# Performance work log

Hardware: AMD Instinct MI355X
Metric: run time of the kernel (lower is better)

## Reference

```python
import jax, jax.numpy as jnp
import numpy as np

TEMP = 2.0   # NTXent uses a hardcoded temperature of 2, not the ctor's 0.07
EPS = 1e-8   # F.cosine_similarity eps


def setup_inputs() -> dict:
    key = jax.random.key(0)
    k1, _ = jax.random.split(key)
    x = jax.random.normal(k1, (8192, 256), dtype=jnp.float32)
    unused = jnp.zeros((1,), dtype=jnp.int32)
    return {"x": x, "unused": unused}


def _cos_matrix(a, b):
    # pairwise cosine similarity: [N, N]
    na = jnp.linalg.norm(a, axis=-1)
    nb = jnp.linalg.norm(b, axis=-1)
    dots = a @ b.T
    return dots / jnp.maximum(na[:, None] * nb[None, :], EPS)


def reference(x, unused):
    n = x.shape[0] // 2
    p, q = x[:n], x[n:]  # anchor, positive

    s_pp = _cos_matrix(p, p)
    s_pn = _cos_matrix(p, q)
    s_nn = _cos_matrix(q, q)
    s_np = _cos_matrix(q, p)

    # double loop i, j in [i, n): upper triangle including diagonal
    mask = jnp.triu(jnp.ones((n, n), dtype=bool))

    exp_sum = (jnp.exp(s_pp / TEMP) + jnp.exp(s_pn / TEMP)
               + jnp.exp(s_nn / TEMP) + jnp.exp(s_np / TEMP))
    sim_all = jnp.sum(jnp.where(mask, exp_sum, 0.0))

    sim_s = jnp.sum(jnp.exp(jnp.diagonal(s_pn) / TEMP))

    return -jnp.log(sim_s / sim_all)
```

## Files before the change

### kernel.cpp

```cpp
#include <hip/hip_runtime.h>

#define DIM    256
#define NROWS  8192
#define NHALF  4096
#define NTILE  64
#define NBLK   ((NTILE * (NTILE + 1)) / 2)

using i32x4  = __attribute__((ext_vector_type(4))) int;
using i32x8  = __attribute__((ext_vector_type(8))) int;
using f32x16 = __attribute__((ext_vector_type(16))) float;

struct i32x8_pair { i32x4 lo, hi; };

__global__ __launch_bounds__(256) void normalize_k(const float* __restrict__ x,
                                                   unsigned char* __restrict__ z8) {
  const int row  = blockIdx.x * 4 + (threadIdx.x >> 6);
  const int lane = threadIdx.x & 63;
  float4 v = ((const float4*)(x + (size_t)row * DIM))[lane];
  float ss = v.x * v.x + v.y * v.y + v.z * v.z + v.w * v.w;
#pragma unroll
  for (int off = 32; off > 0; off >>= 1) ss += __shfl_xor(ss, off, 64);
  float rn = rsqrtf(fmaxf(ss, 1e-24f));
  int p = __builtin_amdgcn_cvt_pk_fp8_f32(v.x * rn, v.y * rn, 0, false);
  p     = __builtin_amdgcn_cvt_pk_fp8_f32(v.z * rn, v.w * rn, p, true);
  ((int*)(z8 + (size_t)row * DIM))[lane] = p;
}

__global__ __launch_bounds__(256, 3) void gram_k(const unsigned char* __restrict__ z8,
                                                 double2* __restrict__ partial) {
  __shared__ unsigned char As[128 * 128];
  __shared__ unsigned char Bs[128 * 128];
  __shared__ float red[8];

  const int bid = blockIdx.x;
  int bi = (int)((129.0 - sqrt(129.0 * 129.0 - 8.0 * (double)bid)) * 0.5);
  while ((bi * (129 - bi)) / 2 > bid) --bi;
  while (((bi + 1) * (128 - bi)) / 2 <= bid) ++bi;
  const int bj = bi + (bid - (bi * (129 - bi)) / 2);

  const int tid   = threadIdx.x;
  const int lane  = tid & 63;
  const int w     = tid >> 6;
  const int wr    = w >> 1, wc = w & 1;
  const int l31   = lane & 31;
  const int khalf = lane >> 5;

  const size_t rowA0 = (size_t)bi * 128;
  const size_t rowB0 = (size_t)bj * 128;

  f32x16 acc_f[2][2] = {};

  for (int kb = 0; kb < 2; ++kb) {
#pragma unroll
    for (int i = 0; i < 4; ++i) {
      int c   = i * 256 + tid;
      int row = c >> 3;
      int cb  = c & 7;
      int gcb = cb ^ (row & 7);
      const unsigned char* ga = z8 + (rowA0 + row) * DIM + kb * 128 + gcb * 16;
      const unsigned char* gb = z8 + (rowB0 + row) * DIM + kb * 128 + gcb * 16;
      __builtin_amdgcn_global_load_lds(
          (const __attribute__((address_space(1))) void*)ga,
          (__attribute__((address_space(3))) void*)&As[(size_t)(i * 256 + (tid & ~63)) * 16],
          16, 0, 0);
      __builtin_amdgcn_global_load_lds(
          (const __attribute__((address_space(1))) void*)gb,
          (__attribute__((address_space(3))) void*)&Bs[(size_t)(i * 256 + (tid & ~63)) * 16],
          16, 0, 0);
    }
    __syncthreads();

#pragma unroll
    for (int kc = 0; kc < 2; ++kc) {
      i32x8 a[2], b[2];
#pragma unroll
      for (int t = 0; t < 2; ++t) {
        const int cb0 = kc * 4 + khalf * 2;
        int mr = wr * 64 + t * 32 + l31;
        i32x8_pair pa = { *(const i32x4*)&As[mr * 128 + ((cb0    ) ^ (mr & 7)) * 16],
                          *(const i32x4*)&As[mr * 128 + ((cb0 + 1) ^ (mr & 7)) * 16] };
        a[t] = __builtin_bit_cast(i32x8, pa);
        int nr = wc * 64 + t * 32 + l31;
        i32x8_pair pb = { *(const i32x4*)&Bs[nr * 128 + ((cb0    ) ^ (nr & 7)) * 16],
                          *(const i32x4*)&Bs[nr * 128 + ((cb0 + 1) ^ (nr & 7)) * 16] };
        b[t] = __builtin_bit_cast(i32x8, pb);
      }
#pragma unroll
      for (int ti = 0; ti < 2; ++ti)
#pragma unroll
        for (int tj = 0; tj < 2; ++tj)
          acc_f[ti][tj] = __builtin_amdgcn_mfma_scale_f32_32x32x64_f8f6f4(
              a[ti], b[tj], acc_f[ti][tj],
              0, 0,
              0, 0x7f7f7f7f,
              0, 0x7f7f7f7f);
    }
    __syncthreads();
  }

  const bool tdiag = (bi == bj);
  const bool sdiag = (bj == bi + 32);
  float lsum = 0.0f, dsum = 0.0f;
  if (tdiag || sdiag) {
#pragma unroll
    for (int ti = 0; ti < 2; ++ti)
#pragma unroll
      for (int tj = 0; tj < 2; ++tj)
#pragma unroll
        for (int r = 0; r < 16; ++r) {
          float e = __expf(acc_f[ti][tj][r] * 0.5f);
          lsum += e;
          int row_l = (r & 3) + 8 * (r >> 2) + 4 * khalf;
          if (wr == wc && ti == tj && row_l == l31) dsum += e;
        }
  } else {
#pragma unroll
    for (int ti = 0; ti < 2; ++ti)
#pragma unroll
      for (int tj = 0; tj < 2; ++tj)
#pragma unroll
        for (int r = 0; r < 16; ++r)
          lsum += __expf(acc_f[ti][tj][r] * 0.5f);
  }
#pragma unroll
  for (int off = 32; off > 0; off >>= 1) lsum += __shfl_xor(lsum, off, 64);
  if (tdiag || sdiag) {
#pragma unroll
    for (int off = 32; off > 0; off >>= 1) dsum += __shfl_xor(dsum, off, 64);
  }
  if (lane == 0) { red[w] = lsum; red[4 + w] = dsum; }
  __syncthreads();

  if (tid == 0) {
    float l  = red[0] + red[1] + red[2] + red[3];
    float dd = red[4] + red[5] + red[6] + red[7];
    double2 v;
    v.x = tdiag ? (double)l + (double)dd : 2.0 * (double)l;
    v.y = sdiag ? (double)dd : 0.0;
    partial[bid] = v;
  }
}

__global__ __launch_bounds__(256) void reduce_k(const double2* __restrict__ partial,
                                                float* __restrict__ out) {
  __shared__ double redS[4], redD[4];
  double s = 0.0, ss = 0.0;
  for (int i = threadIdx.x; i < NBLK; i += 256) {
    double2 v = partial[i];
    s += v.x; ss += v.y;
  }
#pragma unroll
  for (int off = 32; off > 0; off >>= 1) {
    s  += __shfl_xor(s,  off, 64);
    ss += __shfl_xor(ss, off, 64);
  }
  const int w = threadIdx.x >> 6;
  if ((threadIdx.x & 63) == 0) { redS[w] = s; redD[w] = ss; }
  __syncthreads();
  if (threadIdx.x == 0) {
    double S  = redS[0] + redS[1] + redS[2] + redS[3];
    double sd = redD[0] + redD[1] + redD[2] + redD[3];
    out[0] = (float)(log(0.5 * S + sd) - log(sd));
  }
}

extern "C" void kernel_launch(void* const* d_in, const int* in_sizes, int n_in,
                              void* d_out, int out_size, void* d_ws, size_t ws_size,
                              hipStream_t stream) {
  const float* x    = (const float*)d_in[0];
  unsigned char* z8 = (unsigned char*)d_ws;
  double2* partial  = (double2*)((char*)d_ws + (size_t)NROWS * DIM);
  float* out        = (float*)d_out;

  normalize_k<<<dim3(NROWS / 4), dim3(256), 0, stream>>>(x, z8);
  gram_k<<<dim3(NBLK), dim3(256), 0, stream>>>(z8, partial);
  reduce_k<<<dim3(1), dim3(256), 0, stream>>>(partial, out);
}
```

Before: 78.45 us.

## Fuse normalize, gram and reduce into one persistent cooperative kernel

After: 147.5 us. 88.0% more time.

```diff
diff --git a/kernel.cpp b/kernel.cpp
--- a/kernel.cpp
+++ b/kernel.cpp
@@ -1,10 +1,14 @@
 #include <hip/hip_runtime.h>
+#include <hip/hip_cooperative_groups.h>
+
+namespace cg = cooperative_groups;
 
 #define DIM    256
 #define NROWS  8192
 #define NHALF  4096
 #define NTILE  64
 #define NBLK   ((NTILE * (NTILE + 1)) / 2)
+#define MAXGRID 696
 
 using i32x4  = __attribute__((ext_vector_type(4))) int;
 using i32x8  = __attribute__((ext_vector_type(8))) int;
@@ -12,31 +16,15 @@
 
 struct i32x8_pair { i32x4 lo, hi; };
 
-__global__ __launch_bounds__(256) void normalize_k(const float* __restrict__ x,
-                                                   unsigned char* __restrict__ z8) {
-  const int row  = blockIdx.x * 4 + (threadIdx.x >> 6);
-  const int lane = threadIdx.x & 63;
-  float4 v = ((const float4*)(x + (size_t)row * DIM))[lane];
-  float ss = v.x * v.x + v.y * v.y + v.z * v.z + v.w * v.w;
-#pragma unroll
-  for (int off = 32; off > 0; off >>= 1) ss += __shfl_xor(ss, off, 64);
-  float rn = rsqrtf(fmaxf(ss, 1e-24f));
-  int p = __builtin_amdgcn_cvt_pk_fp8_f32(v.x * rn, v.y * rn, 0, false);
-  p     = __builtin_amdgcn_cvt_pk_fp8_f32(v.z * rn, v.w * rn, p, true);
-  ((int*)(z8 + (size_t)row * DIM))[lane] = p;
-}
-
-__global__ __launch_bounds__(256, 3) void gram_k(const unsigned char* __restrict__ z8,
-                                                 double2* __restrict__ partial) {
+__global__ __launch_bounds__(256, 3) void fused_k(const float* __restrict__ x,
+                                                  unsigned char* __restrict__ z8,
+                                                  double2* __restrict__ partial,
+                                                  float* __restrict__ out) {
+  cg::grid_group grid = cg::this_grid();
+
   __shared__ unsigned char As[128 * 128];
   __shared__ unsigned char Bs[128 * 128];
   __shared__ float red[8];
-
-  const int bid = blockIdx.x;
-  int bi = (int)((129.0 - sqrt(129.0 * 129.0 - 8.0 * (double)bid)) * 0.5);
-  while ((bi * (129 - bi)) / 2 > bid) --bi;
-  while (((bi + 1) * (128 - bi)) / 2 <= bid) ++bi;
-  const int bj = bi + (bid - (bi * (129 - bi)) / 2);
 
   const int tid   = threadIdx.x;
   const int lane  = tid & 63;
@@ -45,122 +33,148 @@
   const int l31   = lane & 31;
   const int khalf = lane >> 5;
 
-  const size_t rowA0 = (size_t)bi * 128;
-  const size_t rowB0 = (size_t)bj * 128;
-
-  f32x16 acc_f[2][2] = {};
-
-  for (int kb = 0; kb < 2; ++kb) {
-#pragma unroll
-    for (int i = 0; i < 4; ++i) {
-      int c   = i * 256 + tid;
-      int row = c >> 3;
-      int cb  = c & 7;
-      int gcb = cb ^ (row & 7);
-      const unsigned char* ga = z8 + (rowA0 + row) * DIM + kb * 128 + gcb * 16;
-      const unsigned char* gb = z8 + (rowB0 + row) * DIM + kb * 128 + gcb * 16;
-      __builtin_amdgcn_global_load_lds(
-          (const __attribute__((address_space(1))) void*)ga,
-          (__attribute__((address_space(3))) void*)&As[(size_t)(i * 256 + (tid & ~63)) * 16],
-          16, 0, 0);
-      __builtin_amdgcn_global_load_lds(
-          (const __attribute__((address_space(1))) void*)gb,
-          (__attribute__((address_space(3))) void*)&Bs[(size_t)(i * 256 + (tid & ~63)) * 16],
-          16, 0, 0);
-    }
+  for (int row = blockIdx.x * 4 + w; row < NROWS; row += gridDim.x * 4) {
+    float4 v = ((const float4*)(x + (size_t)row * DIM))[lane];
+    float ss = v.x * v.x + v.y * v.y + v.z * v.z + v.w * v.w;
+#pragma unroll
+    for (int off = 32; off > 0; off >>= 1) ss += __shfl_xor(ss, off, 64);
+    float rn = rsqrtf(fmaxf(ss, 1e-24f));
+    int p = __builtin_amdgcn_cvt_pk_fp8_f32(v.x * rn, v.y * rn, 0, false);
+    p     = __builtin_amdgcn_cvt_pk_fp8_f32(v.z * rn, v.w * rn, p, true);
+    ((int*)(z8 + (size_t)row * DIM))[lane] = p;
+  }
+
+  grid.sync();
+
+  double Sloc = 0.0, ssloc = 0.0;
+  for (int bid = blockIdx.x; bid < NBLK; bid += gridDim.x) {
+    int bi = (int)((129.0 - sqrt(129.0 * 129.0 - 8.0 * (double)bid)) * 0.5);
+    while ((bi * (129 - bi)) / 2 > bid) --bi;
+    while (((bi + 1) * (128 - bi)) / 2 <= bid) ++bi;
+    const int bj = bi + (bid - (bi * (129 - bi)) / 2);
+
+    const size_t rowA0 = (size_t)bi * 128;
+    const size_t rowB0 = (size_t)bj * 128;
+
+    f32x16 acc_f[2][2] = {};
+
+    for (int kb = 0; kb < 2; ++kb) {
+#pragma unroll
+      for (int i = 0; i < 4; ++i) {
+        int c   = i * 256 + tid;
+        int row = c >> 3;
+        int cb  = c & 7;
+        int gcb = cb ^ (row & 7);
+        const unsigned char* ga = z8 + (rowA0 + row) * DIM + kb * 128 + gcb * 16;
+        const unsigned char* gb = z8 + (rowB0 + row) * DIM + kb * 128 + gcb * 16;
+        __builtin_amdgcn_global_load_lds(
+            (const __attribute__((address_space(1))) void*)ga,
+            (__attribute__((address_space(3))) void*)&As[(size_t)(i * 256 + (tid & ~63)) * 16],
+            16, 0, 0);
+        __builtin_amdgcn_global_load_lds(
+            (const __attribute__((address_space(1))) void*)gb,
+            (__attribute__((address_space(3))) void*)&Bs[(size_t)(i * 256 + (tid & ~63)) * 16],
+            16, 0, 0);
+      }
+      __syncthreads();
+
+#pragma unroll
+      for (int kc = 0; kc < 2; ++kc) {
+        i32x8 a[2], b[2];
+#pragma unroll
+        for (int t = 0; t < 2; ++t) {
+          const int cb0 = kc * 4 + khalf * 2;
+          int mr = wr * 64 + t * 32 + l31;
+          i32x8_pair pa = { *(const i32x4*)&As[mr * 128 + ((cb0    ) ^ (mr & 7)) * 16],
+                            *(const i32x4*)&As[mr * 128 + ((cb0 + 1) ^ (mr & 7)) * 16] };
+          a[t] = __builtin_bit_cast(i32x8, pa);
+          int nr = wc * 64 + t * 32 + l31;
+          i32x8_pair pb = { *(const i32x4*)&Bs[nr * 128 + ((cb0    ) ^ (nr & 7)) * 16],
+                            *(const i32x4*)&Bs[nr * 128 + ((cb0 + 1) ^ (nr & 7)) * 16] };
+          b[t] = __builtin_bit_cast(i32x8, pb);
+        }
+#pragma unroll
+        for (int ti = 0; ti < 2; ++ti)
+#pragma unroll
+          for (int tj = 0; tj < 2; ++tj)
+            acc_f[ti][tj] = __builtin_amdgcn_mfma_scale_f32_32x32x64_f8f6f4(
+                a[ti], b[tj], acc_f[ti][tj],
+                0, 0,
+                0, 0x7f7f7f7f,
+                0, 0x7f7f7f7f);
+      }
+      __syncthreads();
+    }
+
+    const bool tdiag = (bi == bj);
+    const bool sdiag = (bj == bi + 32);
+    float lsum = 0.0f, dsum = 0.0f;
+    if (tdiag || sdiag) {
+#pragma unroll
+      for (int ti = 0; ti < 2; ++ti)
+#pragma unroll
+        for (int tj = 0; tj < 2; ++tj)
+#pragma unroll
+          for (int r = 0; r < 16; ++r) {
+            float e = __expf(acc_f[ti][tj][r] * 0.5f);
+            lsum += e;
+            int row_l = (r & 3) + 8 * (r >> 2) + 4 * khalf;
+            if (wr == wc && ti == tj && row_l == l31) dsum += e;
+          }
+    } else {
+#pragma unroll
+      for (int ti = 0; ti < 2; ++ti)
+#pragma unroll
+        for (int tj = 0; tj < 2; ++tj)
+#pragma unroll
+          for (int r = 0; r < 16; ++r)
+            lsum += __expf(acc_f[ti][tj][r] * 0.5f);
+    }
+#pragma unroll
+    for (int off = 32; off > 0; off >>= 1) lsum += __shfl_xor(lsum, off, 64);
+    if (tdiag || sdiag) {
+#pragma unroll
+      for (int off = 32; off > 0; off >>= 1) dsum += __shfl_xor(dsum, off, 64);
+    }
+    if (lane == 0) { red[w] = lsum; red[4 + w] = dsum; }
     __syncthreads();
 
-#pragma unroll
-    for (int kc = 0; kc < 2; ++kc) {
-      i32x8 a[2], b[2];
-#pragma unroll
-      for (int t = 0; t < 2; ++t) {
-        const int cb0 = kc * 4 + khalf * 2;
-        int mr = wr * 64 + t * 32 + l31;
-        i32x8_pair pa = { *(const i32x4*)&As[mr * 128 + ((cb0    ) ^ (mr & 7)) * 16],
-                          *(const i32x4*)&As[mr * 128 + ((cb0 + 1) ^ (mr & 7)) * 16] };
-        a[t] = __builtin_bit_cast(i32x8, pa);
-        int nr = wc * 64 + t * 32 + l31;
-        i32x8_pair pb = { *(const i32x4*)&Bs[nr * 128 + ((cb0    ) ^ (nr & 7)) * 16],
-                          *(const i32x4*)&Bs[nr * 128 + ((cb0 + 1) ^ (nr & 7)) * 16] };
-        b[t] = __builtin_bit_cast(i32x8, pb);
-      }
-#pragma unroll
-      for (int ti = 0; ti < 2; ++ti)
-#pragma unroll
-        for (int tj = 0; tj < 2; ++tj)
-          acc_f[ti][tj] = __builtin_amdgcn_mfma_scale_f32_32x32x64_f8f6f4(
-              a[ti], b[tj], acc_f[ti][tj],
-              0, 0,
-              0, 0x7f7f7f7f,
-              0, 0x7f7f7f7f);
+    if (tid == 0) {
+      float l  = red[0] + red[1] + red[2] + red[3];
+      float dd = red[4] + red[5] + red[6] + red[7];
+      Sloc  += tdiag ? (double)l + (double)dd : 2.0 * (double)l;
+      if (sdiag) ssloc += (double)dd;
     }
     __syncthreads();
   }
 
-  const bool tdiag = (bi == bj);
-  const bool sdiag = (bj == bi + 32);
-  float lsum = 0.0f, dsum = 0.0f;
-  if (tdiag || sdiag) {
-#pragma unroll
-    for (int ti = 0; ti < 2; ++ti)
-#pragma unroll
-      for (int tj = 0; tj < 2; ++tj)
-#pragma unroll
-        for (int r = 0; r < 16; ++r) {
-          float e = __expf(acc_f[ti][tj][r] * 0.5f);
-          lsum += e;
-          int row_l = (r & 3) + 8 * (r >> 2) + 4 * khalf;
-          if (wr == wc && ti == tj && row_l == l31) dsum += e;
-        }
-  } else {
-#pragma unroll
-    for (int ti = 0; ti < 2; ++ti)
-#pragma unroll
-      for (int tj = 0; tj < 2; ++tj)
-#pragma unroll
-        for (int r = 0; r < 16; ++r)
-          lsum += __expf(acc_f[ti][tj][r] * 0.5f);
-  }
-#pragma unroll
-  for (int off = 32; off > 0; off >>= 1) lsum += __shfl_xor(lsum, off, 64);
-  if (tdiag || sdiag) {
-#pragma unroll
-    for (int off = 32; off > 0; off >>= 1) dsum += __shfl_xor(dsum, off, 64);
-  }
-  if (lane == 0) { red[w] = lsum; red[4 + w] = dsum; }
-  __syncthreads();
-
   if (tid == 0) {
-    float l  = red[0] + red[1] + red[2] + red[3];
-    float dd = red[4] + red[5] + red[6] + red[7];
-    double2 v;
-    v.x = tdiag ? (double)l + (double)dd : 2.0 * (double)l;
-    v.y = sdiag ? (double)dd : 0.0;
-    partial[bid] = v;
-  }
-}
-
-__global__ __launch_bounds__(256) void reduce_k(const double2* __restrict__ partial,
-                                                float* __restrict__ out) {
-  __shared__ double redS[4], redD[4];
-  double s = 0.0, ss = 0.0;
-  for (int i = threadIdx.x; i < NBLK; i += 256) {
-    double2 v = partial[i];
-    s += v.x; ss += v.y;
-  }
-#pragma unroll
-  for (int off = 32; off > 0; off >>= 1) {
-    s  += __shfl_xor(s,  off, 64);
-    ss += __shfl_xor(ss, off, 64);
-  }
-  const int w = threadIdx.x >> 6;
-  if ((threadIdx.x & 63) == 0) { redS[w] = s; redD[w] = ss; }
-  __syncthreads();
-  if (threadIdx.x == 0) {
-    double S  = redS[0] + redS[1] + redS[2] + redS[3];
-    double sd = redD[0] + redD[1] + redD[2] + redD[3];
-    out[0] = (float)(log(0.5 * S + sd) - log(sd));
+    double2 v; v.x = Sloc; v.y = ssloc;
+    partial[blockIdx.x] = v;
+  }
+
+  grid.sync();
+
+  if (blockIdx.x == 0) {
+    double* redS = (double*)As;
+    double* redD = (double*)Bs;
+    double s = 0.0, ss = 0.0;
+    for (int i = tid; i < (int)gridDim.x; i += 256) {
+      double2 v = partial[i];
+      s += v.x; ss += v.y;
+    }
+#pragma unroll
+    for (int off = 32; off > 0; off >>= 1) {
+      s  += __shfl_xor(s,  off, 64);
+      ss += __shfl_xor(ss, off, 64);
+    }
+    if (lane == 0) { redS[w] = s; redD[w] = ss; }
+    __syncthreads();
+    if (tid == 0) {
+      double S  = redS[0] + redS[1] + redS[2] + redS[3];
+      double sd = redD[0] + redD[1] + redD[2] + redD[3];
+      out[0] = (float)(log(0.5 * S + sd) - log(sd));
+    }
   }
 }
 
@@ -172,7 +186,17 @@
   double2* partial  = (double2*)((char*)d_ws + (size_t)NROWS * DIM);
   float* out        = (float*)d_out;
 
-  normalize_k<<<dim3(NROWS / 4), dim3(256), 0, stream>>>(x, z8);
-  gram_k<<<dim3(NBLK), dim3(256), 0, stream>>>(z8, partial);
-  reduce_k<<<dim3(1), dim3(256), 0, stream>>>(partial, out);
+  static int grid_blocks = 0;
+  if (grid_blocks == 0) {
+    int nb = 0;
+    if (hipOccupancyMaxActiveBlocksPerMultiprocessor(&nb, (const void*)fused_k,
+                                                     256, 0) != hipSuccess || nb < 1)
+      nb = 1;
+    long cap = (long)nb * 256;
+    grid_blocks = (int)(cap < MAXGRID ? cap : MAXGRID);
+  }
+
+  void* args[] = { (void*)&x, (void*)&z8, (void*)&partial, (void*)&out };
+  hipLaunchCooperativeKernel((void*)fused_k, dim3(grid_blocks), dim3(256),
+                             args, 0, stream);
 }
```

## Give each wave its own 64x64 triangular tile and drop block barriers

Applied to the files above, without the earlier changes.

New measurement: 83.59 us. 6.6% more time.

```diff
diff --git a/kernel.cpp b/kernel.cpp
--- a/kernel.cpp
+++ b/kernel.cpp
@@ -3,8 +3,9 @@
 #define DIM    256
 #define NROWS  8192
 #define NHALF  4096
-#define NTILE  64
-#define NBLK   ((NTILE * (NTILE + 1)) / 2)
+#define NT64   128
+#define NWT    ((NT64 * (NT64 + 1)) / 2)
+#define GRID   (NWT / 4)
 
 using i32x4  = __attribute__((ext_vector_type(4))) int;
 using i32x8  = __attribute__((ext_vector_type(8))) int;
@@ -26,63 +27,61 @@
   ((int*)(z8 + (size_t)row * DIM))[lane] = p;
 }
 
-__global__ __launch_bounds__(256, 3) void gram_k(const unsigned char* __restrict__ z8,
+__global__ __launch_bounds__(256, 2) void gram_k(const unsigned char* __restrict__ z8,
                                                  double2* __restrict__ partial) {
-  __shared__ unsigned char As[128 * 128];
-  __shared__ unsigned char Bs[128 * 128];
-  __shared__ float red[8];
-
-  const int bid = blockIdx.x;
-  int bi = (int)((129.0 - sqrt(129.0 * 129.0 - 8.0 * (double)bid)) * 0.5);
-  while ((bi * (129 - bi)) / 2 > bid) --bi;
-  while (((bi + 1) * (128 - bi)) / 2 <= bid) ++bi;
-  const int bj = bi + (bid - (bi * (129 - bi)) / 2);
+  __shared__ unsigned char buf[4][16384];
+  __shared__ double redS[4], redD[4];
 
   const int tid   = threadIdx.x;
   const int lane  = tid & 63;
   const int w     = tid >> 6;
-  const int wr    = w >> 1, wc = w & 1;
   const int l31   = lane & 31;
   const int khalf = lane >> 5;
 
-  const size_t rowA0 = (size_t)bi * 128;
-  const size_t rowB0 = (size_t)bj * 128;
+  const int id = blockIdx.x * 4 + w;
+  int bi = (int)((257.0 - sqrt(257.0 * 257.0 - 8.0 * (double)id)) * 0.5);
+  while ((bi * (257 - bi)) / 2 > id) --bi;
+  while (((bi + 1) * (256 - bi)) / 2 <= id) ++bi;
+  const int bj = bi + (id - (bi * (257 - bi)) / 2);
+
+  const size_t rowA0 = (size_t)bi * 64;
+  const size_t rowB0 = (size_t)bj * 64;
+
+  unsigned char* Aw = &buf[w][0];
+  unsigned char* Bw = &buf[w][8192];
+
+  const int r8 = lane >> 3;
+  const int c8 = lane & 7;
+  const int sw = c8 ^ r8;
 
   f32x16 acc_f[2][2] = {};
 
   for (int kb = 0; kb < 2; ++kb) {
+    const unsigned char* gA = z8 + (rowA0 + r8) * DIM + kb * 128 + sw * 16;
+    const unsigned char* gB = z8 + (rowB0 + r8) * DIM + kb * 128 + sw * 16;
 #pragma unroll
-    for (int i = 0; i < 4; ++i) {
-      int c   = i * 256 + tid;
-      int row = c >> 3;
-      int cb  = c & 7;
-      int gcb = cb ^ (row & 7);
-      const unsigned char* ga = z8 + (rowA0 + row) * DIM + kb * 128 + gcb * 16;
-      const unsigned char* gb = z8 + (rowB0 + row) * DIM + kb * 128 + gcb * 16;
+    for (int g = 0; g < 8; ++g) {
       __builtin_amdgcn_global_load_lds(
-          (const __attribute__((address_space(1))) void*)ga,
-          (__attribute__((address_space(3))) void*)&As[(size_t)(i * 256 + (tid & ~63)) * 16],
-          16, 0, 0);
+          (const __attribute__((address_space(1))) void*)(gA + (size_t)g * 8 * DIM),
+          (__attribute__((address_space(3))) void*)(Aw + g * 1024), 16, 0, 0);
       __builtin_amdgcn_global_load_lds(
-          (const __attribute__((address_space(1))) void*)gb,
-          (__attribute__((address_space(3))) void*)&Bs[(size_t)(i * 256 + (tid & ~63)) * 16],
-          16, 0, 0);
+          (const __attribute__((address_space(1))) void*)(gB + (size_t)g * 8 * DIM),
+          (__attribute__((address_space(3))) void*)(Bw + g * 1024), 16, 0, 0);
     }
-    __syncthreads();
+    __asm__ __volatile__("s_waitcnt vmcnt(0)" ::: "memory");
 
 #pragma unroll
     for (int kc = 0; kc < 2; ++kc) {
+      const int cb0 = kc * 4 + khalf * 2;
       i32x8 a[2], b[2];
 #pragma unroll
       for (int t = 0; t < 2; ++t) {
-        const int cb0 = kc * 4 + khalf * 2;
-        int mr = wr * 64 + t * 32 + l31;
-        i32x8_pair pa = { *(const i32x4*)&As[mr * 128 + ((cb0    ) ^ (mr & 7)) * 16],
-                          *(const i32x4*)&As[mr * 128 + ((cb0 + 1) ^ (mr & 7)) * 16] };
+        int r = t * 32 + l31;
+        i32x8_pair pa = { *(const i32x4*)&Aw[r * 128 + ((cb0    ) ^ (r & 7)) * 16],
+                          *(const i32x4*)&Aw[r * 128 + ((cb0 + 1) ^ (r & 7)) * 16] };
         a[t] = __builtin_bit_cast(i32x8, pa);
-        int nr = wc * 64 + t * 32 + l31;
-        i32x8_pair pb = { *(const i32x4*)&Bs[nr * 128 + ((cb0    ) ^ (nr & 7)) * 16],
-                          *(const i32x4*)&Bs[nr * 128 + ((cb0 + 1) ^ (nr & 7)) * 16] };
+        i32x8_pair pb = { *(const i32x4*)&Bw[r * 128 + ((cb0    ) ^ (r & 7)) * 16],
+                          *(const i32x4*)&Bw[r * 128 + ((cb0 + 1) ^ (r & 7)) * 16] };
         b[t] = __builtin_bit_cast(i32x8, pb);
       }
 #pragma unroll
@@ -95,11 +94,11 @@
               0, 0x7f7f7f7f,
               0, 0x7f7f7f7f);
     }
-    __syncthreads();
+    __asm__ __volatile__("s_waitcnt lgkmcnt(0)" ::: "memory");
   }
 
   const bool tdiag = (bi == bj);
-  const bool sdiag = (bj == bi + 32);
+  const bool sdiag = (bj == bi + 64);
   float lsum = 0.0f, dsum = 0.0f;
   if (tdiag || sdiag) {
 #pragma unroll
@@ -111,7 +110,7 @@
           float e = __expf(acc_f[ti][tj][r] * 0.5f);
           lsum += e;
           int row_l = (r & 3) + 8 * (r >> 2) + 4 * khalf;
-          if (wr == wc && ti == tj && row_l == l31) dsum += e;
+          if (ti == tj && row_l == l31) dsum += e;
         }
   } else {
 #pragma unroll
@@ -128,16 +127,17 @@
 #pragma unroll
     for (int off = 32; off > 0; off >>= 1) dsum += __shfl_xor(dsum, off, 64);
   }
-  if (lane == 0) { red[w] = lsum; red[4 + w] = dsum; }
+
+  if (lane == 0) {
+    redS[w] = tdiag ? (double)lsum + (double)dsum : 2.0 * (double)lsum;
+    redD[w] = sdiag ? (double)dsum : 0.0;
+  }
   __syncthreads();
-
   if (tid == 0) {
-    float l  = red[0] + red[1] + red[2] + red[3];
-    float dd = red[4] + red[5] + red[6] + red[7];
     double2 v;
-    v.x = tdiag ? (double)l + (double)dd : 2.0 * (double)l;
-    v.y = sdiag ? (double)dd : 0.0;
-    partial[bid] = v;
+    v.x = redS[0] + redS[1] + redS[2] + redS[3];
+    v.y = redD[0] + redD[1] + redD[2] + redD[3];
+    partial[blockIdx.x] = v;
   }
 }
 
@@ -145,7 +145,7 @@
                                                 float* __restrict__ out) {
   __shared__ double redS[4], redD[4];
   double s = 0.0, ss = 0.0;
-  for (int i = threadIdx.x; i < NBLK; i += 256) {
+  for (int i = threadIdx.x; i < GRID; i += 256) {
     double2 v = partial[i];
     s += v.x; ss += v.y;
   }
@@ -173,6 +173,6 @@
   float* out        = (float*)d_out;
 
   normalize_k<<<dim3(NROWS / 4), dim3(256), 0, stream>>>(x, z8);
-  gram_k<<<dim3(NBLK), dim3(256), 0, stream>>>(z8, partial);
+  gram_k<<<dim3(GRID), dim3(256), 0, stream>>>(z8, partial);
   reduce_k<<<dim3(1), dim3(256), 0, stream>>>(partial, out);
 }
```

## Quantize normalized rows to FP4 and run Gram matrix with FP4 MFMA

Applied to the files above, without the earlier changes.

Result: faster. 75.20 us (-4.1%).

```diff
diff --git a/kernel.cpp b/kernel.cpp
--- a/kernel.cpp
+++ b/kernel.cpp
@@ -5,6 +5,7 @@
 #define NHALF  4096
 #define NTILE  64
 #define NBLK   ((NTILE * (NTILE + 1)) / 2)
+#define RSTRIDE 128
 
 using i32x4  = __attribute__((ext_vector_type(4))) int;
 using i32x8  = __attribute__((ext_vector_type(8))) int;
@@ -12,24 +13,33 @@
 
 struct i32x8_pair { i32x4 lo, hi; };
 
+__device__ __forceinline__ unsigned fp4q(float v) {
+  float a = fabsf(v);
+  unsigned s = (__builtin_bit_cast(unsigned, v) >> 31) << 3;
+  unsigned c = a < 0.25f ? 0u : a < 0.75f ? 1u : a < 1.25f ? 2u : a < 1.75f ? 3u
+             : a < 2.50f ? 4u : a < 3.50f ? 5u : a < 5.00f ? 6u : 7u;
+  return s | c;
+}
+
 __global__ __launch_bounds__(256) void normalize_k(const float* __restrict__ x,
-                                                   unsigned char* __restrict__ z8) {
+                                                   unsigned char* __restrict__ z4) {
   const int row  = blockIdx.x * 4 + (threadIdx.x >> 6);
   const int lane = threadIdx.x & 63;
   float4 v = ((const float4*)(x + (size_t)row * DIM))[lane];
   float ss = v.x * v.x + v.y * v.y + v.z * v.z + v.w * v.w;
 #pragma unroll
   for (int off = 32; off > 0; off >>= 1) ss += __shfl_xor(ss, off, 64);
-  float rn = rsqrtf(fmaxf(ss, 1e-24f));
-  int p = __builtin_amdgcn_cvt_pk_fp8_f32(v.x * rn, v.y * rn, 0, false);
-  p     = __builtin_amdgcn_cvt_pk_fp8_f32(v.z * rn, v.w * rn, p, true);
-  ((int*)(z8 + (size_t)row * DIM))[lane] = p;
+  float rn = rsqrtf(fmaxf(ss, 1e-24f)) * 16.0f;
+  unsigned c0 = fp4q(v.x * rn), c1 = fp4q(v.y * rn);
+  unsigned c2 = fp4q(v.z * rn), c3 = fp4q(v.w * rn);
+  unsigned short pk = (unsigned short)((c0 | (c1 << 4)) | ((c2 | (c3 << 4)) << 8));
+  ((unsigned short*)(z4 + (size_t)row * RSTRIDE))[lane] = pk;
 }
 
-__global__ __launch_bounds__(256, 3) void gram_k(const unsigned char* __restrict__ z8,
+__global__ __launch_bounds__(256, 4) void gram_k(const unsigned char* __restrict__ z4,
                                                  double2* __restrict__ partial) {
-  __shared__ unsigned char As[128 * 128];
-  __shared__ unsigned char Bs[128 * 128];
+  __shared__ unsigned char As[128 * RSTRIDE];
+  __shared__ unsigned char Bs[128 * RSTRIDE];
   __shared__ float red[8];
 
   const int bid = blockIdx.x;
@@ -48,54 +58,49 @@
   const size_t rowA0 = (size_t)bi * 128;
   const size_t rowB0 = (size_t)bj * 128;
 
+#pragma unroll
+  for (int i = 0; i < 4; ++i) {
+    int c   = i * 256 + tid;
+    int row = c >> 3;
+    int cb  = c & 7;
+    int gcb = cb ^ (row & 7);
+    const unsigned char* ga = z4 + (rowA0 + row) * RSTRIDE + gcb * 16;
+    const unsigned char* gb = z4 + (rowB0 + row) * RSTRIDE + gcb * 16;
+    __builtin_amdgcn_global_load_lds(
+        (const __attribute__((address_space(1))) void*)ga,
+        (__attribute__((address_space(3))) void*)&As[(size_t)(i * 256 + (tid & ~63)) * 16],
+        16, 0, 0);
+    __builtin_amdgcn_global_load_lds(
+        (const __attribute__((address_space(1))) void*)gb,
+        (__attribute__((address_space(3))) void*)&Bs[(size_t)(i * 256 + (tid & ~63)) * 16],
+        16, 0, 0);
+  }
+  __syncthreads();
+
   f32x16 acc_f[2][2] = {};
-
-  for (int kb = 0; kb < 2; ++kb) {
+  const i32x4 zero4 = {0, 0, 0, 0};
 #pragma unroll
-    for (int i = 0; i < 4; ++i) {
-      int c   = i * 256 + tid;
-      int row = c >> 3;
-      int cb  = c & 7;
-      int gcb = cb ^ (row & 7);
-      const unsigned char* ga = z8 + (rowA0 + row) * DIM + kb * 128 + gcb * 16;
-      const unsigned char* gb = z8 + (rowB0 + row) * DIM + kb * 128 + gcb * 16;
-      __builtin_amdgcn_global_load_lds(
-          (const __attribute__((address_space(1))) void*)ga,
-          (__attribute__((address_space(3))) void*)&As[(size_t)(i * 256 + (tid & ~63)) * 16],
-          16, 0, 0);
-      __builtin_amdgcn_global_load_lds(
-          (const __attribute__((address_space(1))) void*)gb,
-          (__attribute__((address_space(3))) void*)&Bs[(size_t)(i * 256 + (tid & ~63)) * 16],
-          16, 0, 0);
+  for (int kc = 0; kc < 4; ++kc) {
+    const int ch = kc * 2 + khalf;
+    i32x8 a[2], b[2];
+#pragma unroll
+    for (int t = 0; t < 2; ++t) {
+      int mr = wr * 64 + t * 32 + l31;
+      i32x8_pair pa = { *(const i32x4*)&As[mr * RSTRIDE + (ch ^ (mr & 7)) * 16], zero4 };
+      a[t] = __builtin_bit_cast(i32x8, pa);
+      int nr = wc * 64 + t * 32 + l31;
+      i32x8_pair pb = { *(const i32x4*)&Bs[nr * RSTRIDE + (ch ^ (nr & 7)) * 16], zero4 };
+      b[t] = __builtin_bit_cast(i32x8, pb);
     }
-    __syncthreads();
-
 #pragma unroll
-    for (int kc = 0; kc < 2; ++kc) {
-      i32x8 a[2], b[2];
+    for (int ti = 0; ti < 2; ++ti)
 #pragma unroll
-      for (int t = 0; t < 2; ++t) {
-        const int cb0 = kc * 4 + khalf * 2;
-        int mr = wr * 64 + t * 32 + l31;
-        i32x8_pair pa = { *(const i32x4*)&As[mr * 128 + ((cb0    ) ^ (mr & 7)) * 16],
-                          *(const i32x4*)&As[mr * 128 + ((cb0 + 1) ^ (mr & 7)) * 16] };
-        a[t] = __builtin_bit_cast(i32x8, pa);
-        int nr = wc * 64 + t * 32 + l31;
-        i32x8_pair pb = { *(const i32x4*)&Bs[nr * 128 + ((cb0    ) ^ (nr & 7)) * 16],
-                          *(const i32x4*)&Bs[nr * 128 + ((cb0 + 1) ^ (nr & 7)) * 16] };
-        b[t] = __builtin_bit_cast(i32x8, pb);
-      }
-#pragma unroll
-      for (int ti = 0; ti < 2; ++ti)
-#pragma unroll
-        for (int tj = 0; tj < 2; ++tj)
-          acc_f[ti][tj] = __builtin_amdgcn_mfma_scale_f32_32x32x64_f8f6f4(
-              a[ti], b[tj], acc_f[ti][tj],
-              0, 0,
-              0, 0x7f7f7f7f,
-              0, 0x7f7f7f7f);
-    }
-    __syncthreads();
+      for (int tj = 0; tj < 2; ++tj)
+        acc_f[ti][tj] = __builtin_amdgcn_mfma_scale_f32_32x32x64_f8f6f4(
+            a[ti], b[tj], acc_f[ti][tj],
+            4, 4,
+            0, 0x7B7B7B7B,
+            0, 0x7B7B7B7B);
   }
 
   const bool tdiag = (bi == bj);
@@ -142,7 +147,7 @@
 }
 
 __global__ __launch_bounds__(256) void reduce_k(const double2* __restrict__ partial,
-                                                float* __restrict__ out) {
+                                               float* __restrict__ out) {
   __shared__ double redS[4], redD[4];
   double s = 0.0, ss = 0.0;
   for (int i = threadIdx.x; i < NBLK; i += 256) {
@@ -168,11 +173,11 @@
                               void* d_out, int out_size, void* d_ws, size_t ws_size,
                               hipStream_t stream) {
   const float* x    = (const float*)d_in[0];
-  unsigned char* z8 = (unsigned char*)d_ws;
-  double2* partial  = (double2*)((char*)d_ws + (size_t)NROWS * DIM);
+  unsigned char* z4 = (unsigned char*)d_ws;
+  double2* partial  = (double2*)((char*)d_ws + (size_t)NROWS * RSTRIDE);
   float* out        = (float*)d_out;
 
-  normalize_k<<<dim3(NROWS / 4), dim3(256), 0, stream>>>(x, z8);
-  gram_k<<<dim3(NBLK), dim3(256), 0, stream>>>(z8, partial);
+  normalize_k<<<dim3(NROWS / 4), dim3(256), 0, stream>>>(x, z4);
+  gram_k<<<dim3(NBLK), dim3(256), 0, stream>>>(z4, partial);
   reduce_k<<<dim3(1), dim3(256), 0, stream>>>(partial, out);
 }
```
